# Performance work log

Measured on AMD Instinct MI355X. Metric: run time of the kernel, lower is better.

The kernel has to match this reference:

```python
import jax, jax.numpy as jnp
import numpy as np

B, S, H, E, K, DFF = 4, 2048, 1024, 8, 2, 4096


def setup_inputs() -> dict:
    key = jax.random.key(0)
    k0, k1, k2, k3 = jax.random.split(key, 4)
    sc = 0.02
    return {
        "x": jax.random.normal(k0, (B, S, H), jnp.float32),
        "gate_W": jax.random.normal(k1, (H, E), jnp.float32) * sc,
        "gate_b": jnp.zeros((E,), jnp.float32),
        "W1": jax.random.normal(k2, (H, DFF), jnp.float32) * sc,
        "b1": jnp.zeros((DFF,), jnp.float32),
        "W2": jax.random.normal(k3, (DFF, H), jnp.float32) * sc,
        "b2": jnp.zeros((H,), jnp.float32),
    }


def reference(x, gate_W, gate_b, W1, b1, W2, b2):
    b, s, h = x.shape
    x_flat = x.reshape(-1, h)                      # [T, H]
    gate_scores = x_flat @ gate_W + gate_b         # [T, E]
    top_k_scores, top_k_idx = jax.lax.top_k(gate_scores, K)   # [T, K]
    top_k_w = jax.nn.softmax(top_k_scores, axis=-1)           # [T, K]

    # All experts share the same weights (ModuleList reuses one module), so
    # sum_i w_i * expert_i(x) == expert(x) * sum_i w_i. top_k indices are
    # unique per token, so the per-token combine weight is sum of top-k weights.
    hdd = jax.nn.gelu(x_flat @ W1 + b1, approximate=False)    # [T, DFF]
    y = hdd @ W2 + b2                                         # [T, H]
    tok_w = top_k_w.sum(axis=-1)                              # [T] (== 1.0)
    output = (y * tok_w[:, None]).reshape(b, s, h)

    expert_load = gate_scores.mean(axis=0)                    # [E]
    aux_loss = (expert_load ** 2).sum()
    exp_counts = jnp.zeros((E,), jnp.int32).at[top_k_idx.ravel()].add(1)
    return output, aux_loss, exp_counts
```

## Files before the change

### kernel.cpp

```cpp
#include <hip/hip_runtime.h>
#include <hip/hip_bf16.h>
#include <math.h>

#define Tn   8192
#define Hn   1024
#define En   8
#define DFFn 4096

typedef __attribute__((ext_vector_type(8))) short bf16x8;
typedef __attribute__((ext_vector_type(8))) unsigned short u16x8;
typedef __attribute__((ext_vector_type(4))) float f32x4;

static __device__ inline unsigned short f2bf(float f) {
    __hip_bfloat16 h = __float2bfloat16(f);
    return __builtin_bit_cast(unsigned short, h);
}

__global__ __launch_bounds__(256) void prep(
    const float* __restrict__ W1, unsigned short* __restrict__ W1t,
    const float* __restrict__ W2, unsigned short* __restrict__ W2t,
    const float* __restrict__ x, const float* __restrict__ gW,
    const float* __restrict__ gb, unsigned short* __restrict__ xbf,
    float* __restrict__ tokw, float* __restrict__ load_sum,
    int* __restrict__ counts)
{
    __shared__ float smem[8 * 1024 + En];
    __shared__ int   s_cnt[En];
    const int tid = threadIdx.x;
    const int id  = blockIdx.x;

    if (id < 512) {
        const float* src; unsigned short* dst; int SR, SC, tb;
        if (id < 256) { src = W1; dst = W1t; SR = Hn;   SC = DFFn; tb = id; }
        else          { src = W2; dst = W2t; SR = DFFn; SC = Hn;   tb = id - 256; }
        const int tcs = SC >> 7;
        const int tr  = tb / tcs, tc = tb - tr * tcs;
        const int r0  = tr << 7, c0 = tc << 7;
        unsigned short* tile = (unsigned short*)smem;

        #pragma unroll
        for (int i = 0; i < 16; ++i) {
            int idx = tid + i * 256;
            int r = idx >> 5, c4 = (idx & 31) << 2;
            float4 v = *(const float4*)(src + (size_t)(r0 + r) * SC + c0 + c4);
            int cs = c4 ^ (((r >> 3) & 7) << 2);
            ushort4 pk;
            pk.x = f2bf(v.x); pk.y = f2bf(v.y);
            pk.z = f2bf(v.z); pk.w = f2bf(v.w);
            *(ushort4*)(tile + r * 128 + cs) = pk;
        }
        __syncthreads();
        #pragma unroll
        for (int i = 0; i < 8; ++i) {
            int idx = tid + i * 256;
            int n = idx >> 4, kg = idx & 15, k0 = kg << 3;
            int s = (kg & 7) << 2;
            u16x8 o;
            #pragma unroll
            for (int j = 0; j < 8; ++j)
                o[j] = tile[(k0 + j) * 128 + (n ^ s)];
            *(u16x8*)(dst + (size_t)(c0 + n) * SR + r0 + k0) = o;
        }
        return;
    }

    const int gid = id - 512;
    float* gwt    = smem;
    float* s_load = smem + 8 * 1024;
    if (tid < En) { s_load[tid] = 0.f; s_cnt[tid] = 0; }
    #pragma unroll
    for (int i = 0; i < 32; ++i) {
        int f = tid + i * 256;
        gwt[(f & 7) * 1024 + (f >> 3)] = gW[f];
    }
    __syncthreads();

    const int lane = tid & 63;
    const int wv   = tid >> 6;

    for (int tok = gid * 4 + wv; tok < Tn; tok += 4096) {
        const float4* xr = (const float4*)(x + (size_t)tok * Hn);
        float acc[8] = {0.f,0.f,0.f,0.f,0.f,0.f,0.f,0.f};
        #pragma unroll
        for (int j = 0; j < Hn / 256; ++j) {
            int h4 = j * 64 + lane;
            float4 xv = xr[h4];
            ushort4 pk;
            pk.x = f2bf(xv.x); pk.y = f2bf(xv.y);
            pk.z = f2bf(xv.z); pk.w = f2bf(xv.w);
            ((ushort4*)xbf)[(size_t)tok * (Hn / 4) + h4] = pk;
            #pragma unroll
            for (int e = 0; e < 8; ++e) {
                const float4 w = *(const float4*)(gwt + e * 1024 + h4 * 4);
                acc[e] += xv.x * w.x + xv.y * w.y + xv.z * w.z + xv.w * w.w;
            }
        }
        #pragma unroll
        for (int e = 0; e < 8; ++e) {
            float v = acc[e];
            #pragma unroll
            for (int off = 32; off > 0; off >>= 1) v += __shfl_xor(v, off, 64);
            acc[e] = v + gb[e];
        }
        if (lane == 0) {
            #pragma unroll
            for (int e = 0; e < 8; ++e) atomicAdd(&s_load[e], acc[e]);
            int i1 = 0; float v1 = acc[0];
            #pragma unroll
            for (int e = 1; e < 8; ++e) if (acc[e] > v1) { v1 = acc[e]; i1 = e; }
            int i2 = -1; float v2 = -3.0e38f;
            #pragma unroll
            for (int e = 0; e < 8; ++e) if (e != i1 && acc[e] > v2) { v2 = acc[e]; i2 = e; }
            atomicAdd(&s_cnt[i1], 1);
            atomicAdd(&s_cnt[i2], 1);
            float e2 = __expf(v2 - v1);
            float t  = 1.0f + e2;
            tokw[tok] = 1.0f / t + e2 / t;
        }
    }
    __syncthreads();
    if (tid < En) {
        atomicAdd(&load_sum[tid], s_load[tid]);
        atomicAdd(&counts[tid],   s_cnt[tid]);
    }
}

static __device__ inline bf16x8 ldsfrag(const char* base, int row, int chunk) {
    return *(const bf16x8*)(base + row * 128 + (((chunk) ^ (row & 7)) << 4));
}

template<int BN, int WM, int WN, int EPI>
__global__ __launch_bounds__(512, 2) void gemm8(
    const __hip_bfloat16* __restrict__ A,
    const __hip_bfloat16* __restrict__ Bt,
    const float* __restrict__ bias,
    const float* __restrict__ tokw,
    void* __restrict__ C, int N, int K, int nx,
    const float* __restrict__ load_sum, const int* __restrict__ counts,
    float* __restrict__ out_tail, int nblk)
{
    constexpr int BM = 256;
    constexpr int MR = (BM / WM) / 16;
    constexpr int NR = (BN / WN) / 16;
    constexpr int AU = BM / 64;
    constexpr int BU = BN / 64;
    constexpr int ABYTES = BM * 64 * 2;
    constexpr int BBYTES = BN * 64 * 2;
    constexpr int TILEB  = ABYTES + BBYTES;

    extern __shared__ char lds[];

    const int tid = threadIdx.x;
    const int id  = blockIdx.x;

    if (EPI == 0 && id >= nblk) {
        if (tid == 0) {
            float aux = 0.f;
            #pragma unroll
            for (int e = 0; e < En; ++e) {
                float m = load_sum[e] * (1.0f / (float)Tn);
                aux += m * m;
            }
            out_tail[0] = aux;
            #pragma unroll
            for (int e = 0; e < En; ++e) out_tail[1 + e] = (float)counts[e];
        }
        return;
    }

    int wg = id;
    { int xcd = wg & 7, idx = wg >> 3; wg = xcd * (nblk >> 3) + idx; }
    const int by = wg / nx, bx = wg % nx;
    const int m0 = by * BM, n0 = bx * BN;

    const int lane = tid & 63;
    const int wid  = tid >> 6;
    const int wn   = wid % WN;
    const int wm   = wid / WN;
    const int wrow = wm * (BM / WM);
    const int wcol = wn * (BN / WN);
    const int fr   = lane & 15;
    const int fq   = lane >> 4;

    const int sr = tid >> 3;
    const int sc = (tid & 7) ^ (sr & 7);
    unsigned aOff[AU], bOff[BU];
    #pragma unroll
    for (int u = 0; u < AU; ++u)
        aOff[u] = (unsigned)((m0 + u * 64 + sr) * K + sc * 8);
    #pragma unroll
    for (int u = 0; u < BU; ++u)
        bOff[u] = (unsigned)((n0 + u * 64 + sr) * K + sc * 8);

#define STA(b, u, kt) __builtin_amdgcn_global_load_lds( \
    (const __attribute__((address_space(1))) void*)(A + aOff[u] + (unsigned)(kt) * 64u), \
    (__attribute__((address_space(3))) void*)(lds + (b) * TILEB + (u) * 8192 + tid * 16), 16, 0, 0)
#define STB(b, u, kt) __builtin_amdgcn_global_load_lds( \
    (const __attribute__((address_space(1))) void*)(Bt + bOff[u] + (unsigned)(kt) * 64u), \
    (__attribute__((address_space(3))) void*)(lds + (b) * TILEB + ABYTES + (u) * 8192 + tid * 16), 16, 0, 0)

    bf16x8 af[MR / 2][2];
    bf16x8 bfr[4][2];
    f32x4  acc[MR][NR];
    const f32x4 zero = {0.f, 0.f, 0.f, 0.f};
    #pragma unroll
    for (int i = 0; i < MR; ++i)
        #pragma unroll
        for (int j = 0; j < NR; ++j) acc[i][j] = zero;

#define RD_A1(b, half, m_) do { _Pragma("unroll") \
    for (int ks_ = 0; ks_ < 2; ++ks_) \
        af[m_][ks_] = ldsfrag(lds + (b) * TILEB, \
            wrow + ((half) * (MR / 2) + (m_)) * 16 + fr, ks_ * 4 + fq); } while (0)
#define RD_B1(b, nn) do { _Pragma("unroll") \
    for (int ks_ = 0; ks_ < 2; ++ks_) \
        bfr[nn][ks_] = ldsfrag(lds + (b) * TILEB + ABYTES, \
            wcol + (nn) * 16 + fr, ks_ * 4 + fq); } while (0)

#define MFMA_M(hm, hn, m_) do { _Pragma("unroll") \
    for (int n_ = 0; n_ < 2; ++n_) { _Pragma("unroll") \
        for (int ks_ = 0; ks_ < 2; ++ks_) \
            acc[(hm) * (MR / 2) + (m_)][(hn) * 2 + n_] = \
                __builtin_amdgcn_mfma_f32_16x16x32_bf16( \
                    af[m_][ks_], bfr[(hn) * 2 + n_][ks_], \
                    acc[(hm) * (MR / 2) + (m_)][(hn) * 2 + n_], 0, 0, 0); } } while (0)
#define MFMA_N(hm, nn) do { _Pragma("unroll") \
    for (int m_ = 0; m_ < MR / 2; ++m_) { _Pragma("unroll") \
        for (int ks_ = 0; ks_ < 2; ++ks_) \
            acc[(hm) * (MR / 2) + m_][nn] = \
                __builtin_amdgcn_mfma_f32_16x16x32_bf16( \
                    af[m_][ks_], bfr[nn][ks_], \
                    acc[(hm) * (MR / 2) + m_][nn], 0, 0, 0); } } while (0)

#define MFMA1_N(hm, nn) do { _Pragma("unroll") \
    for (int m_ = 0; m_ < MR / 2; ++m_) { _Pragma("unroll") \
        for (int ks_ = 0; ks_ < 2; ++ks_) \
            acc[(hm) * (MR / 2) + m_][nn] = \
                __builtin_amdgcn_mfma_f32_16x16x32_bf16( \
                    bfr[nn][ks_], af[m_][ks_], \
                    acc[(hm) * (MR / 2) + m_][nn], 0, 0, 0); } } while (0)
#define MFMA1_M(hm, m_) do { _Pragma("unroll") \
    for (int n_ = 0; n_ < NR; ++n_) { _Pragma("unroll") \
        for (int ks_ = 0; ks_ < 2; ++ks_) \
            acc[(hm) * (MR / 2) + (m_)][n_] = \
                __builtin_amdgcn_mfma_f32_16x16x32_bf16( \
                    bfr[n_][ks_], af[m_][ks_], \
                    acc[(hm) * (MR / 2) + (m_)][n_], 0, 0, 0); } } while (0)

#define SBAR do { \
    __builtin_amdgcn_sched_barrier(0); \
    __builtin_amdgcn_s_barrier(); \
    __builtin_amdgcn_sched_barrier(0); } while (0)
#define WAITL(n) do { \
    asm volatile("s_waitcnt lgkmcnt(" #n ")" ::: "memory"); \
    __builtin_amdgcn_sched_barrier(0); } while (0)
#define PRIO1 __builtin_amdgcn_s_setprio(1)
#define PRIO0 __builtin_amdgcn_s_setprio(0)
#define DRAIN6 do { asm volatile("s_waitcnt vmcnt(6)" ::: "memory"); \
    __builtin_amdgcn_sched_barrier(0); } while (0)
#define DRAIN2 do { asm volatile("s_waitcnt vmcnt(2)" ::: "memory"); \
    __builtin_amdgcn_sched_barrier(0); } while (0)

    const int KT = K >> 6;

    if constexpr (WM == 2) {
        STA(0,0,0); STA(0,1,0); STA(0,2,0); STA(0,3,0);
        STB(0,0,0); STB(0,1,0); STB(0,2,0); STB(0,3,0);
        STA(1,0,1); STA(1,2,1);
        STB(1,0,1); STB(1,1,1); STB(1,2,1); STB(1,3,1);
        DRAIN6;
        __builtin_amdgcn_s_barrier();
        __builtin_amdgcn_sched_barrier(0);

        for (int i = 0; i < (KT >> 1); ++i) {
            const int t1 = 2 * i + 1;
            const int c2 = (2 * i + 2 < KT) ? 2 * i + 2 : KT - 1;
            const int c3 = (2 * i + 3 < KT) ? 2 * i + 3 : KT - 1;

            RD_B1(0,0); RD_B1(0,1);
            RD_A1(0,0,0); RD_A1(0,0,1); RD_A1(0,0,2); RD_A1(0,0,3);
            STA(1,1,t1); STA(1,3,t1);
            SBAR; PRIO1;
            WAITL(6); MFMA_M(0,0,0);
            WAITL(4); MFMA_M(0,0,1);
            WAITL(2); MFMA_M(0,0,2);
            WAITL(0); MFMA_M(0,0,3);
            PRIO0; SBAR;
            RD_B1(0,2); RD_B1(0,3);
            STA(0,0,c2); STA(0,2,c2);
            SBAR; PRIO1;
            WAITL(2); MFMA_N(0,2);
            WAITL(0); MFMA_N(0,3);
            PRIO0; SBAR;
            RD_A1(0,1,0); RD_A1(0,1,1); RD_A1(0,1,2); RD_A1(0,1,3);
            STB(0,0,c2); STB(0,1,c2);
            SBAR; PRIO1;
            WAITL(6); MFMA_M(1,0,0);
            WAITL(4); MFMA_M(1,0,1);
            WAITL(2); MFMA_M(1,0,2);
            WAITL(0); MFMA_M(1,0,3);
            PRIO0; SBAR;
            STB(0,2,c2); STB(0,3,c2);
            SBAR; PRIO1;
            MFMA_M(1,1,0); MFMA_M(1,1,1); MFMA_M(1,1,2); MFMA_M(1,1,3);
            PRIO0; DRAIN6; SBAR;
            RD_B1(1,0); RD_B1(1,1);
            RD_A1(1,0,0); RD_A1(1,0,1); RD_A1(1,0,2); RD_A1(1,0,3);
            STA(0,1,c2); STA(0,3,c2);
            SBAR; PRIO1;
            WAITL(6); MFMA_M(0,0,0);
            WAITL(4); MFMA_M(0,0,1);
            WAITL(2); MFMA_M(0,0,2);
            WAITL(0); MFMA_M(0,0,3);
            PRIO0; SBAR;
            RD_B1(1,2); RD_B1(1,3);
            STA(1,0,c3); STA(1,2,c3);
            SBAR; PRIO1;
            WAITL(2); MFMA_N(0,2);
            WAITL(0); MFMA_N(0,3);
            PRIO0; SBAR;
            RD_A1(1,1,0); RD_A1(1,1,1); RD_A1(1,1,2); RD_A1(1,1,3);
            STB(1,0,c3); STB(1,1,c3);
            SBAR; PRIO1;
            WAITL(6); MFMA_M(1,0,0);
            WAITL(4); MFMA_M(1,0,1);
            WAITL(2); MFMA_M(1,0,2);
            WAITL(0); MFMA_M(1,0,3);
            PRIO0; SBAR;
            STB(1,2,c3); STB(1,3,c3);
            SBAR; PRIO1;
            MFMA_M(1,1,0); MFMA_M(1,1,1); MFMA_M(1,1,2); MFMA_M(1,1,3);
            PRIO0; DRAIN6; SBAR;
        }

        float bias4[NR];
        #pragma unroll
        for (int ni = 0; ni < NR; ++ni)
            bias4[ni] = bias[n0 + wcol + ni * 16 + fr];
        #pragma unroll
        for (int mi = 0; mi < MR; ++mi) {
            #pragma unroll
            for (int ni = 0; ni < NR; ++ni) {
                const int col = n0 + wcol + ni * 16 + fr;
                const int rb  = m0 + wrow + mi * 16 + fq * 4;
                #pragma unroll
                for (int i2 = 0; i2 < 4; ++i2) {
                    float u  = acc[mi][ni][i2] + bias4[ni];
                    float uu = u * u;
                    float z  = u * __fmaf_rn(uu, -0.07135607f, -1.59576912f);
                    float e  = __expf(z);
                    float g  = u * __builtin_amdgcn_rcpf(1.0f + e);
                    ((__hip_bfloat16*)C)[(size_t)(rb + i2) * N + col] =
                        __float2bfloat16(g);
                }
            }
        }
    } else {
        STA(0,0,0); STA(0,1,0); STA(0,2,0); STA(0,3,0);
        STB(0,0,0); STB(0,1,0);
        STB(1,0,1); STB(1,1,1);
        DRAIN2;
        __builtin_amdgcn_s_barrier();
        __builtin_amdgcn_sched_barrier(0);

        for (int i = 0; i < (KT >> 1); ++i) {
            const int t1 = 2 * i + 1;
            const int c2 = (2 * i + 2 < KT) ? 2 * i + 2 : KT - 1;
            const int c3 = (2 * i + 3 < KT) ? 2 * i + 3 : KT - 1;

            RD_A1(0,0,0); RD_A1(0,0,1);
            RD_B1(0,0); RD_B1(0,1); RD_B1(0,2); RD_B1(0,3);
            STA(1,0,t1); STA(1,1,t1); STA(1,2,t1); STA(1,3,t1);
            SBAR; PRIO1;
            WAITL(6); MFMA1_N(0,0);
            WAITL(4); MFMA1_N(0,1);
            WAITL(2); MFMA1_N(0,2);
            WAITL(0); MFMA1_N(0,3);
            PRIO0; SBAR;
            RD_A1(0,1,0); RD_A1(0,1,1);
            STB(0,0,c2); STB(0,1,c2);
            SBAR; PRIO1;
            WAITL(2); MFMA1_M(1,0);
            WAITL(0); MFMA1_M(1,1);
            PRIO0; DRAIN2; SBAR;
            RD_A1(1,0,0); RD_A1(1,0,1);
            RD_B1(1,0); RD_B1(1,1); RD_B1(1,2); RD_B1(1,3);
            STA(0,0,c2); STA(0,1,c2); STA(0,2,c2); STA(0,3,c2);
            SBAR; PRIO1;
            WAITL(6); MFMA1_N(0,0);
            WAITL(4); MFMA1_N(0,1);
            WAITL(2); MFMA1_N(0,2);
            WAITL(0); MFMA1_N(0,3);
            PRIO0; SBAR;
            RD_A1(1,1,0); RD_A1(1,1,1);
            STB(1,0,c3); STB(1,1,c3);
            SBAR; PRIO1;
            WAITL(2); MFMA1_M(1,0);
            WAITL(0); MFMA1_M(1,1);
            PRIO0; DRAIN2; SBAR;
        }

        const int mrow0 = m0 + wrow + fr;
        const int ncol0 = n0 + wcol + fq * 4;
        float4 b4[NR];
        #pragma unroll
        for (int ni = 0; ni < NR; ++ni)
            b4[ni] = *(const float4*)(bias + ncol0 + ni * 16);

        #pragma unroll
        for (int mi = 0; mi < MR; ++mi) {
            const int row = mrow0 + mi * 16;
            const float tw = tokw[row];
            #pragma unroll
            for (int ni = 0; ni < NR; ++ni) {
                f32x4 v = acc[mi][ni];
                float4 o;
                o.x = (v[0] + b4[ni].x) * tw;
                o.y = (v[1] + b4[ni].y) * tw;
                o.z = (v[2] + b4[ni].z) * tw;
                o.w = (v[3] + b4[ni].w) * tw;
                *(float4*)((float*)C + (size_t)row * N + ncol0 + ni * 16) = o;
            }
        }
    }

#undef STA
#undef STB
#undef RD_A1
#undef RD_B1
#undef MFMA_M
#undef MFMA_N
#undef MFMA1_N
#undef MFMA1_M
#undef SBAR
#undef WAITL
#undef PRIO1
#undef PRIO0
#undef DRAIN6
#undef DRAIN2
}

extern "C" void kernel_launch(void* const* d_in, const int* in_sizes, int n_in,
                              void* d_out, int out_size, void* d_ws, size_t ws_size,
                              hipStream_t stream)
{
    const float* x  = (const float*)d_in[0];
    const float* gW = (const float*)d_in[1];
    const float* gb = (const float*)d_in[2];
    const float* W1 = (const float*)d_in[3];
    const float* b1 = (const float*)d_in[4];
    const float* W2 = (const float*)d_in[5];
    const float* b2 = (const float*)d_in[6];
    float* out = (float*)d_out;

    char* ws = (char*)d_ws;
    __hip_bfloat16* xbf = (__hip_bfloat16*)ws;  ws += (size_t)Tn * Hn * 2;
    __hip_bfloat16* W1t = (__hip_bfloat16*)ws;  ws += (size_t)Hn * DFFn * 2;
    __hip_bfloat16* W2t = (__hip_bfloat16*)ws;  ws += (size_t)Hn * DFFn * 2;
    __hip_bfloat16* hdd = (__hip_bfloat16*)ws;  ws += (size_t)Tn * DFFn * 2;
    float* tokw     = (float*)ws;               ws += (size_t)Tn * 4;
    float* load_sum = (float*)ws;               ws += En * 4;
    int*   counts   = (int*)ws;                 ws += En * 4;

    static bool attr_done = false;
    if (!attr_done) {
        (void)hipFuncSetAttribute(
            reinterpret_cast<const void*>(&gemm8<256, 2, 4, 0>),
            hipFuncAttributeMaxDynamicSharedMemorySize, 131072);
        (void)hipFuncSetAttribute(
            reinterpret_cast<const void*>(&gemm8<128, 4, 2, 1>),
            hipFuncAttributeMaxDynamicSharedMemorySize, 98304);
        attr_done = true;
    }

    hipMemsetAsync(load_sum, 0, En * 4 * 2, stream);

    prep<<<1536, 256, 0, stream>>>(W1, (unsigned short*)W1t,
                                   W2, (unsigned short*)W2t,
                                   x, gW, gb, (unsigned short*)xbf,
                                   tokw, load_sum, counts);

    gemm8<256, 2, 4, 0><<<513, 512, 131072, stream>>>(
        xbf, W1t, b1, nullptr, hdd, DFFn, Hn, 16,
        load_sum, counts, out + (size_t)Tn * Hn, 512);

    gemm8<128, 4, 2, 1><<<256, 512, 98304, stream>>>(
        hdd, W2t, b2, tokw, out, Hn, DFFn, 8,
        nullptr, nullptr, nullptr, 256);
}
```

Before: 267.7 us.

## Restructure GEMM main loops with coarser MFMA phases and register double-buffered fragments

Both GEMM variants (the W1 GEMM with GELU and the W2 GEMM with the weighted output) get a rewritten inner schedule. LDS fragment reads are issued one phase ahead, with ping-pong fragment registers in the second kernel. The many fine-grained lgkmcnt waits are replaced by fewer, larger MFMA blocks, and the vmcnt drain points move. The goal is to hide LDS read latency behind MFMA work and cut barrier and wait overhead. The cost is more live registers, which could lower occupancy or cause spills, and the hand-tuned waitcnt values could be wrong.

```diff
diff --git a/kernel.cpp b/kernel.cpp
--- a/kernel.cpp
+++ b/kernel.cpp
@@ -199,54 +199,6 @@
     (const __attribute__((address_space(1))) void*)(Bt + bOff[u] + (unsigned)(kt) * 64u), \
     (__attribute__((address_space(3))) void*)(lds + (b) * TILEB + ABYTES + (u) * 8192 + tid * 16), 16, 0, 0)
 
-    bf16x8 af[MR / 2][2];
-    bf16x8 bfr[4][2];
-    f32x4  acc[MR][NR];
-    const f32x4 zero = {0.f, 0.f, 0.f, 0.f};
-    #pragma unroll
-    for (int i = 0; i < MR; ++i)
-        #pragma unroll
-        for (int j = 0; j < NR; ++j) acc[i][j] = zero;
-
-#define RD_A1(b, half, m_) do { _Pragma("unroll") \
-    for (int ks_ = 0; ks_ < 2; ++ks_) \
-        af[m_][ks_] = ldsfrag(lds + (b) * TILEB, \
-            wrow + ((half) * (MR / 2) + (m_)) * 16 + fr, ks_ * 4 + fq); } while (0)
-#define RD_B1(b, nn) do { _Pragma("unroll") \
-    for (int ks_ = 0; ks_ < 2; ++ks_) \
-        bfr[nn][ks_] = ldsfrag(lds + (b) * TILEB + ABYTES, \
-            wcol + (nn) * 16 + fr, ks_ * 4 + fq); } while (0)
-
-#define MFMA_M(hm, hn, m_) do { _Pragma("unroll") \
-    for (int n_ = 0; n_ < 2; ++n_) { _Pragma("unroll") \
-        for (int ks_ = 0; ks_ < 2; ++ks_) \
-            acc[(hm) * (MR / 2) + (m_)][(hn) * 2 + n_] = \
-                __builtin_amdgcn_mfma_f32_16x16x32_bf16( \
-                    af[m_][ks_], bfr[(hn) * 2 + n_][ks_], \
-                    acc[(hm) * (MR / 2) + (m_)][(hn) * 2 + n_], 0, 0, 0); } } while (0)
-#define MFMA_N(hm, nn) do { _Pragma("unroll") \
-    for (int m_ = 0; m_ < MR / 2; ++m_) { _Pragma("unroll") \
-        for (int ks_ = 0; ks_ < 2; ++ks_) \
-            acc[(hm) * (MR / 2) + m_][nn] = \
-                __builtin_amdgcn_mfma_f32_16x16x32_bf16( \
-                    af[m_][ks_], bfr[nn][ks_], \
-                    acc[(hm) * (MR / 2) + m_][nn], 0, 0, 0); } } while (0)
-
-#define MFMA1_N(hm, nn) do { _Pragma("unroll") \
-    for (int m_ = 0; m_ < MR / 2; ++m_) { _Pragma("unroll") \
-        for (int ks_ = 0; ks_ < 2; ++ks_) \
-            acc[(hm) * (MR / 2) + m_][nn] = \
-                __builtin_amdgcn_mfma_f32_16x16x32_bf16( \
-                    bfr[nn][ks_], af[m_][ks_], \
-                    acc[(hm) * (MR / 2) + m_][nn], 0, 0, 0); } } while (0)
-#define MFMA1_M(hm, m_) do { _Pragma("unroll") \
-    for (int n_ = 0; n_ < NR; ++n_) { _Pragma("unroll") \
-        for (int ks_ = 0; ks_ < 2; ++ks_) \
-            acc[(hm) * (MR / 2) + (m_)][n_] = \
-                __builtin_amdgcn_mfma_f32_16x16x32_bf16( \
-                    bfr[n_][ks_], af[m_][ks_], \
-                    acc[(hm) * (MR / 2) + (m_)][n_], 0, 0, 0); } } while (0)
-
 #define SBAR do { \
     __builtin_amdgcn_sched_barrier(0); \
     __builtin_amdgcn_s_barrier(); \
@@ -254,93 +206,92 @@
 #define WAITL(n) do { \
     asm volatile("s_waitcnt lgkmcnt(" #n ")" ::: "memory"); \
     __builtin_amdgcn_sched_barrier(0); } while (0)
+#define VMC(n) do { asm volatile("s_waitcnt vmcnt(" #n ")" ::: "memory"); \
+    __builtin_amdgcn_sched_barrier(0); } while (0)
 #define PRIO1 __builtin_amdgcn_s_setprio(1)
 #define PRIO0 __builtin_amdgcn_s_setprio(0)
-#define DRAIN6 do { asm volatile("s_waitcnt vmcnt(6)" ::: "memory"); \
-    __builtin_amdgcn_sched_barrier(0); } while (0)
-#define DRAIN2 do { asm volatile("s_waitcnt vmcnt(2)" ::: "memory"); \
-    __builtin_amdgcn_sched_barrier(0); } while (0)
 
     const int KT = K >> 6;
 
     if constexpr (WM == 2) {
+        bf16x8 af[4][2];
+        bf16x8 bfr[4][2];
+        f32x4  acc[8][4];
+        const f32x4 zero = {0.f, 0.f, 0.f, 0.f};
+        #pragma unroll
+        for (int i = 0; i < 8; ++i)
+            #pragma unroll
+            for (int j = 0; j < 4; ++j) acc[i][j] = zero;
+
+#define RD_A(b, half) do { _Pragma("unroll") \
+    for (int m_ = 0; m_ < 4; ++m_) { _Pragma("unroll") \
+        for (int ks_ = 0; ks_ < 2; ++ks_) \
+            af[m_][ks_] = ldsfrag(lds + (b) * TILEB, \
+                wrow + ((half) * 4 + m_) * 16 + fr, ks_ * 4 + fq); } } while (0)
+#define RD_B(b, nn) do { _Pragma("unroll") \
+    for (int ks_ = 0; ks_ < 2; ++ks_) \
+        bfr[nn][ks_] = ldsfrag(lds + (b) * TILEB + ABYTES, \
+            wcol + (nn) * 16 + fr, ks_ * 4 + fq); } while (0)
+#define MFMAQ(hm, hn) do { \
+    PRIO1; \
+    _Pragma("unroll") \
+    for (int m_ = 0; m_ < 4; ++m_) { _Pragma("unroll") \
+        for (int n_ = 0; n_ < 2; ++n_) { _Pragma("unroll") \
+            for (int ks_ = 0; ks_ < 2; ++ks_) \
+                acc[(hm) * 4 + m_][(hn) * 2 + n_] = \
+                    __builtin_amdgcn_mfma_f32_16x16x32_bf16( \
+                        af[m_][ks_], bfr[(hn) * 2 + n_][ks_], \
+                        acc[(hm) * 4 + m_][(hn) * 2 + n_], 0, 0, 0); } } \
+    PRIO0; } while (0)
+
         STA(0,0,0); STA(0,1,0); STA(0,2,0); STA(0,3,0);
         STB(0,0,0); STB(0,1,0); STB(0,2,0); STB(0,3,0);
         STA(1,0,1); STA(1,2,1);
         STB(1,0,1); STB(1,1,1); STB(1,2,1); STB(1,3,1);
-        DRAIN6;
+        VMC(6);
         __builtin_amdgcn_s_barrier();
         __builtin_amdgcn_sched_barrier(0);
+        RD_B(0,0); RD_B(0,1);
 
         for (int i = 0; i < (KT >> 1); ++i) {
             const int t1 = 2 * i + 1;
             const int c2 = (2 * i + 2 < KT) ? 2 * i + 2 : KT - 1;
             const int c3 = (2 * i + 3 < KT) ? 2 * i + 3 : KT - 1;
 
-            RD_B1(0,0); RD_B1(0,1);
-            RD_A1(0,0,0); RD_A1(0,0,1); RD_A1(0,0,2); RD_A1(0,0,3);
+            RD_A(0,0);
+            RD_B(0,2); RD_B(0,3);
             STA(1,1,t1); STA(1,3,t1);
-            SBAR; PRIO1;
-            WAITL(6); MFMA_M(0,0,0);
-            WAITL(4); MFMA_M(0,0,1);
-            WAITL(2); MFMA_M(0,0,2);
-            WAITL(0); MFMA_M(0,0,3);
-            PRIO0; SBAR;
-            RD_B1(0,2); RD_B1(0,3);
+            SBAR; WAITL(4); MFMAQ(0,0); SBAR;
             STA(0,0,c2); STA(0,2,c2);
-            SBAR; PRIO1;
-            WAITL(2); MFMA_N(0,2);
-            WAITL(0); MFMA_N(0,3);
-            PRIO0; SBAR;
-            RD_A1(0,1,0); RD_A1(0,1,1); RD_A1(0,1,2); RD_A1(0,1,3);
+            SBAR; WAITL(0); MFMAQ(0,1); SBAR;
+            RD_A(0,1);
             STB(0,0,c2); STB(0,1,c2);
-            SBAR; PRIO1;
-            WAITL(6); MFMA_M(1,0,0);
-            WAITL(4); MFMA_M(1,0,1);
-            WAITL(2); MFMA_M(1,0,2);
-            WAITL(0); MFMA_M(1,0,3);
-            PRIO0; SBAR;
+            SBAR; WAITL(0); MFMAQ(1,0); VMC(4); SBAR;
+            RD_B(1,0); RD_B(1,1);
             STB(0,2,c2); STB(0,3,c2);
-            SBAR; PRIO1;
-            MFMA_M(1,1,0); MFMA_M(1,1,1); MFMA_M(1,1,2); MFMA_M(1,1,3);
-            PRIO0; DRAIN6; SBAR;
-            RD_B1(1,0); RD_B1(1,1);
-            RD_A1(1,0,0); RD_A1(1,0,1); RD_A1(1,0,2); RD_A1(1,0,3);
+            SBAR; WAITL(4); MFMAQ(1,1); SBAR;
+            RD_A(1,0);
+            RD_B(1,2); RD_B(1,3);
             STA(0,1,c2); STA(0,3,c2);
-            SBAR; PRIO1;
-            WAITL(6); MFMA_M(0,0,0);
-            WAITL(4); MFMA_M(0,0,1);
-            WAITL(2); MFMA_M(0,0,2);
-            WAITL(0); MFMA_M(0,0,3);
-            PRIO0; SBAR;
-            RD_B1(1,2); RD_B1(1,3);
+            SBAR; WAITL(4); MFMAQ(0,0); SBAR;
             STA(1,0,c3); STA(1,2,c3);
-            SBAR; PRIO1;
-            WAITL(2); MFMA_N(0,2);
-            WAITL(0); MFMA_N(0,3);
-            PRIO0; SBAR;
-            RD_A1(1,1,0); RD_A1(1,1,1); RD_A1(1,1,2); RD_A1(1,1,3);
+            SBAR; WAITL(0); MFMAQ(0,1); SBAR;
+            RD_A(1,1);
             STB(1,0,c3); STB(1,1,c3);
-            SBAR; PRIO1;
-            WAITL(6); MFMA_M(1,0,0);
-            WAITL(4); MFMA_M(1,0,1);
-            WAITL(2); MFMA_M(1,0,2);
-            WAITL(0); MFMA_M(1,0,3);
-            PRIO0; SBAR;
+            SBAR; WAITL(0); MFMAQ(1,0); VMC(4); SBAR;
+            RD_B(0,0); RD_B(0,1);
             STB(1,2,c3); STB(1,3,c3);
-            SBAR; PRIO1;
-            MFMA_M(1,1,0); MFMA_M(1,1,1); MFMA_M(1,1,2); MFMA_M(1,1,3);
-            PRIO0; DRAIN6; SBAR;
-        }
-
-        float bias4[NR];
-        #pragma unroll
-        for (int ni = 0; ni < NR; ++ni)
+            SBAR; WAITL(4); MFMAQ(1,1); SBAR;
+        }
+
+        float bias4[4];
+        #pragma unroll
+        for (int ni = 0; ni < 4; ++ni)
             bias4[ni] = bias[n0 + wcol + ni * 16 + fr];
         #pragma unroll
-        for (int mi = 0; mi < MR; ++mi) {
-            #pragma unroll
-            for (int ni = 0; ni < NR; ++ni) {
+        for (int mi = 0; mi < 8; ++mi) {
+            #pragma unroll
+            for (int ni = 0; ni < 4; ++ni) {
                 const int col = n0 + wcol + ni * 16 + fr;
                 const int rb  = m0 + wrow + mi * 16 + fq * 4;
                 #pragma unroll
@@ -355,64 +306,81 @@
                 }
             }
         }
+#undef RD_A
+#undef RD_B
+#undef MFMAQ
     } else {
+        bf16x8 afh0[2][2], afh1[2][2];
+        bf16x8 bfrS0[4][2], bfrS1[4][2];
+        f32x4  acc[4][4];
+        const f32x4 zero = {0.f, 0.f, 0.f, 0.f};
+        #pragma unroll
+        for (int i = 0; i < 4; ++i)
+            #pragma unroll
+            for (int j = 0; j < 4; ++j) acc[i][j] = zero;
+
+#define RD_AH(dst, b, half) do { _Pragma("unroll") \
+    for (int m_ = 0; m_ < 2; ++m_) { _Pragma("unroll") \
+        for (int ks_ = 0; ks_ < 2; ++ks_) \
+            dst[m_][ks_] = ldsfrag(lds + (b) * TILEB, \
+                wrow + ((half) * 2 + m_) * 16 + fr, ks_ * 4 + fq); } } while (0)
+#define RD_BS(dst, b) do { _Pragma("unroll") \
+    for (int n_ = 0; n_ < 4; ++n_) { _Pragma("unroll") \
+        for (int ks_ = 0; ks_ < 2; ++ks_) \
+            dst[n_][ks_] = ldsfrag(lds + (b) * TILEB + ABYTES, \
+                wcol + n_ * 16 + fr, ks_ * 4 + fq); } } while (0)
+#define MFMAH(afx, bfx, hm) do { \
+    PRIO1; \
+    _Pragma("unroll") \
+    for (int m_ = 0; m_ < 2; ++m_) { _Pragma("unroll") \
+        for (int n_ = 0; n_ < 4; ++n_) { _Pragma("unroll") \
+            for (int ks_ = 0; ks_ < 2; ++ks_) \
+                acc[(hm) * 2 + m_][n_] = \
+                    __builtin_amdgcn_mfma_f32_16x16x32_bf16( \
+                        bfx[n_][ks_], afx[m_][ks_], \
+                        acc[(hm) * 2 + m_][n_], 0, 0, 0); } } \
+    PRIO0; } while (0)
+
         STA(0,0,0); STA(0,1,0); STA(0,2,0); STA(0,3,0);
         STB(0,0,0); STB(0,1,0);
         STB(1,0,1); STB(1,1,1);
-        DRAIN2;
+        STA(1,0,1); STA(1,1,1); STA(1,2,1); STA(1,3,1);
+        VMC(6);
         __builtin_amdgcn_s_barrier();
         __builtin_amdgcn_sched_barrier(0);
+        RD_AH(afh0, 0, 0); RD_BS(bfrS0, 0);
 
         for (int i = 0; i < (KT >> 1); ++i) {
-            const int t1 = 2 * i + 1;
             const int c2 = (2 * i + 2 < KT) ? 2 * i + 2 : KT - 1;
             const int c3 = (2 * i + 3 < KT) ? 2 * i + 3 : KT - 1;
 
-            RD_A1(0,0,0); RD_A1(0,0,1);
-            RD_B1(0,0); RD_B1(0,1); RD_B1(0,2); RD_B1(0,3);
-            STA(1,0,t1); STA(1,1,t1); STA(1,2,t1); STA(1,3,t1);
-            SBAR; PRIO1;
-            WAITL(6); MFMA1_N(0,0);
-            WAITL(4); MFMA1_N(0,1);
-            WAITL(2); MFMA1_N(0,2);
-            WAITL(0); MFMA1_N(0,3);
-            PRIO0; SBAR;
-            RD_A1(0,1,0); RD_A1(0,1,1);
+            RD_AH(afh1, 0, 1);
+            SBAR; WAITL(0); MFMAH(afh0, bfrS0, 0); VMC(0); SBAR;
+            RD_AH(afh0, 1, 0); RD_BS(bfrS1, 1);
             STB(0,0,c2); STB(0,1,c2);
-            SBAR; PRIO1;
-            WAITL(2); MFMA1_M(1,0);
-            WAITL(0); MFMA1_M(1,1);
-            PRIO0; DRAIN2; SBAR;
-            RD_A1(1,0,0); RD_A1(1,0,1);
-            RD_B1(1,0); RD_B1(1,1); RD_B1(1,2); RD_B1(1,3);
             STA(0,0,c2); STA(0,1,c2); STA(0,2,c2); STA(0,3,c2);
-            SBAR; PRIO1;
-            WAITL(6); MFMA1_N(0,0);
-            WAITL(4); MFMA1_N(0,1);
-            WAITL(2); MFMA1_N(0,2);
-            WAITL(0); MFMA1_N(0,3);
-            PRIO0; SBAR;
-            RD_A1(1,1,0); RD_A1(1,1,1);
+            SBAR; WAITL(12); MFMAH(afh1, bfrS0, 1); SBAR;
+            RD_AH(afh1, 1, 1);
+            SBAR; WAITL(0); MFMAH(afh0, bfrS1, 0); VMC(0); SBAR;
+            RD_AH(afh0, 0, 0); RD_BS(bfrS0, 0);
             STB(1,0,c3); STB(1,1,c3);
-            SBAR; PRIO1;
-            WAITL(2); MFMA1_M(1,0);
-            WAITL(0); MFMA1_M(1,1);
-            PRIO0; DRAIN2; SBAR;
+            STA(1,0,c3); STA(1,1,c3); STA(1,2,c3); STA(1,3,c3);
+            SBAR; WAITL(12); MFMAH(afh1, bfrS1, 1); SBAR;
         }
 
         const int mrow0 = m0 + wrow + fr;
         const int ncol0 = n0 + wcol + fq * 4;
-        float4 b4[NR];
-        #pragma unroll
-        for (int ni = 0; ni < NR; ++ni)
+        float4 b4[4];
+        #pragma unroll
+        for (int ni = 0; ni < 4; ++ni)
             b4[ni] = *(const float4*)(bias + ncol0 + ni * 16);
 
         #pragma unroll
-        for (int mi = 0; mi < MR; ++mi) {
+        for (int mi = 0; mi < 4; ++mi) {
             const int row = mrow0 + mi * 16;
             const float tw = tokw[row];
             #pragma unroll
-            for (int ni = 0; ni < NR; ++ni) {
+            for (int ni = 0; ni < 4; ++ni) {
                 f32x4 v = acc[mi][ni];
                 float4 o;
                 o.x = (v[0] + b4[ni].x) * tw;
@@ -422,22 +390,18 @@
                 *(float4*)((float*)C + (size_t)row * N + ncol0 + ni * 16) = o;
             }
         }
+#undef RD_AH
+#undef RD_BS
+#undef MFMAH
     }
 
 #undef STA
 #undef STB
-#undef RD_A1
-#undef RD_B1
-#undef MFMA_M
-#undef MFMA_N
-#undef MFMA1_N
-#undef MFMA1_M
 #undef SBAR
 #undef WAITL
+#undef VMC
 #undef PRIO1
 #undef PRIO0
-#undef DRAIN6
-#undef DRAIN2
 }
 
 extern "C" void kernel_launch(void* const* d_in, const int* in_sizes, int n_in,
```

After: 268.7 us. About the same (+0.4%).
